# Optimization experiments

Hardware: AMD Instinct MI355X
Metric: run time of the kernel (lower is better)

The kernel has to match this reference:

```python
import jax, jax.numpy as jnp
import numpy as np

N = 10000          # nodes
E = 320000         # edges (avg degree 32)
D_IN = 64          # node_pos feature width
NS, NG, NV = 128, 128, 128   # gate: scalars, gates, gated channels
NTYPES = 8         # edge types
FC = 64            # fc_neurons hidden width
D_OUT = 64
NUM_NEIGHBORS = 32.0


def setup_inputs() -> dict:
    key = jax.random.key(0)
    ks = jax.random.split(key, 32)
    inp = {}
    inp["node_pos"] = jax.random.normal(ks[0], (N, D_IN), dtype=jnp.float32)
    dims_in = [D_IN, D_IN + NS + NV, D_IN + NS + NV]     # 64, 320, 320
    dims_out = [NS + NG + NV, NS + NG + NV, D_OUT]       # 384, 384, 64
    i = 1
    for l in range(3):
        di, do = dims_in[l], dims_out[l]
        inp[f"w_self_{l}"] = jax.random.normal(ks[i], (di, do), dtype=jnp.float32) / np.sqrt(di); i += 1
        inp[f"w_msg_{l}"] = jax.random.normal(ks[i], (di, do), dtype=jnp.float32) / np.sqrt(di); i += 1
        inp[f"fc0_{l}"] = jax.random.normal(ks[i], (NTYPES, FC), dtype=jnp.float32) / np.sqrt(NTYPES); i += 1
        inp[f"fc1_{l}"] = jax.random.normal(ks[i], (FC, FC), dtype=jnp.float32) / np.sqrt(FC); i += 1
        inp[f"fc2_{l}"] = jax.random.normal(ks[i], (FC, do), dtype=jnp.float32) / np.sqrt(FC); i += 1
    inp["edge_src"] = jax.random.randint(ks[i], (E,), 0, N); i += 1
    inp["edge_dst"] = jax.random.randint(ks[i], (E,), 0, N); i += 1
    inp["edge_type"] = jax.random.randint(ks[i], (E,), 0, NTYPES)
    return inp


def _conv(x, edge_src, edge_dst, etype_onehot, w_self, w_msg, f0, f1, f2):
    # fc_neurons MLP on edge attrs -> per-edge tensor-product weights [E, out]
    w = jax.nn.silu(etype_onehot @ f0)
    w = jax.nn.silu(w @ f1)
    w = w @ f2
    # gather source node features, weighted message, scatter-sum to dst
    msg = (x[edge_src] @ w_msg) * w                       # [E, out]
    agg = jax.ops.segment_sum(msg, edge_dst, num_segments=N)
    agg = agg / jnp.sqrt(jnp.asarray(NUM_NEIGHBORS, x.dtype))
    return x @ w_self + agg                               # self-connection + messages


def _gate(h):
    # e3nn Gate: scalars -> silu, gates -> sigmoid, gated channels modulated by gates
    s = h[:, :NS]
    g = h[:, NS:NS + NG]
    v = h[:, NS + NG:]
    return jnp.concatenate([jax.nn.silu(s), v * jax.nn.sigmoid(g)], axis=-1)


def reference(node_pos,
              w_self_0, w_msg_0, fc0_0, fc1_0, fc2_0,
              w_self_1, w_msg_1, fc0_1, fc1_1, fc2_1,
              w_self_2, w_msg_2, fc0_2, fc1_2, fc2_2,
              edge_src, edge_dst, edge_type):
    etype_onehot = jax.nn.one_hot(edge_type, NTYPES, dtype=node_pos.dtype)
    mid = node_pos
    params = [(w_self_0, w_msg_0, fc0_0, fc1_0, fc2_0),
              (w_self_1, w_msg_1, fc0_1, fc1_1, fc2_1)]
    for w_self, w_msg, f0, f1, f2 in params:
        h = _conv(mid, edge_src, edge_dst, etype_onehot, w_self, w_msg, f0, f1, f2)
        mid = jnp.concatenate([node_pos, _gate(h)], axis=-1)   # concated_tensor
    return _conv(mid, edge_src, edge_dst, etype_onehot, w_self_2, w_msg_2, fc0_2, fc1_2, fc2_2)
```

## Files before the change

### kernel.cpp

```cpp
#include <hip/hip_runtime.h>
#include <hip/hip_bf16.h>

#define N_NODES 10000
#define N_EDGES 320000
#define NTYPES 8
#define FC 64
#define SLOTS 96

using short8v = __attribute__((ext_vector_type(8))) short;
using f32x4   = __attribute__((ext_vector_type(4))) float;

__device__ __forceinline__ float sigmoidf_(float x) { return 1.f / (1.f + expf(-x)); }

__device__ __forceinline__ unsigned short f2bf(float x) {
    union { float f; unsigned u; } un; un.f = x;
    unsigned r = un.u + 0x7fff + ((un.u >> 16) & 1);
    return (unsigned short)(r >> 16);
}
__device__ __forceinline__ float bflo(unsigned d) {
    union { unsigned u; float f; } un; un.u = d << 16; return un.f;
}
__device__ __forceinline__ float bfhi(unsigned d) {
    union { unsigned u; float f; } un; un.u = d & 0xffff0000u; return un.f;
}
__device__ __forceinline__ unsigned packbf(float lo, float hi) {
    return (unsigned)f2bf(lo) | ((unsigned)f2bf(hi) << 16);
}

__device__ __forceinline__ void wtrans(const float* __restrict__ in,
                                       unsigned short* __restrict__ out,
                                       int K, int Nn, int idx) {
    int n = idx / K, k = idx - n * K;
    out[idx] = f2bf(in[k * Nn + n]);
}

#define PREP_TOTAL (N_NODES + N_NODES * 64 + 2 * 24576 + 2 * 122880 + 2 * 20480)

__global__ void prep_all(const float* __restrict__ node_pos,
                         const float* __restrict__ w0, const float* __restrict__ w1,
                         const float* __restrict__ w2, const float* __restrict__ w3,
                         const float* __restrict__ w4, const float* __restrict__ w5,
                         const float* __restrict__ f0_0, const float* __restrict__ f1_0,
                         const float* __restrict__ f2_0,
                         const float* __restrict__ f0_1, const float* __restrict__ f1_1,
                         const float* __restrict__ f2_1,
                         const float* __restrict__ f0_2, const float* __restrict__ f1_2,
                         const float* __restrict__ f2_2,
                         int* __restrict__ cnt, unsigned short* __restrict__ np16,
                         unsigned short* __restrict__ o0, unsigned short* __restrict__ o1,
                         unsigned short* __restrict__ o2, unsigned short* __restrict__ o3,
                         unsigned short* __restrict__ o4, unsigned short* __restrict__ o5,
                         float* __restrict__ wtab0, float* __restrict__ wtab1,
                         float* __restrict__ wtab2) {
    const int tid = threadIdx.x;
    const int bb = blockIdx.x;
    if (bb < 26) {
        const float *f0, *f1, *f2;
        float* wtab;
        int dout, idx;
        if (bb < 12)      { f0 = f0_0; f1 = f1_0; f2 = f2_0; wtab = wtab0; dout = 384; idx = bb * 256 + tid; }
        else if (bb < 24) { f0 = f0_1; f1 = f1_1; f2 = f2_1; wtab = wtab1; dout = 384; idx = (bb - 12) * 256 + tid; }
        else              { f0 = f0_2; f1 = f1_2; f2 = f2_2; wtab = wtab2; dout = 64;  idx = (bb - 24) * 256 + tid; }
        __shared__ float a[NTYPES * FC];
        __shared__ float bs[NTYPES * FC];
        for (int i = tid; i < NTYPES * FC; i += 256) { float v = f0[i]; a[i] = v * sigmoidf_(v); }
        __syncthreads();
        for (int i = tid; i < NTYPES * FC; i += 256) {
            int t = i >> 6, j = i & 63;
            float s = 0.f;
            #pragma unroll
            for (int k = 0; k < FC; ++k) s = fmaf(a[t * FC + k], f1[k * FC + j], s);
            bs[i] = s * sigmoidf_(s);
        }
        __syncthreads();
        if (idx >= NTYPES * dout) return;
        int t = idx / dout, c = idx - t * dout;
        float s = 0.f;
        #pragma unroll
        for (int k = 0; k < FC; ++k) s = fmaf(bs[t * FC + k], f2[k * dout + c], s);
        wtab[idx] = s * 0.17677669529663687f;
        return;
    }
    int idx = (bb - 26) * 256 + tid;
    if (idx < N_NODES) { cnt[idx] = 0; return; }
    idx -= N_NODES;
    if (idx < N_NODES * 64) { np16[idx] = f2bf(node_pos[idx]); return; }
    idx -= N_NODES * 64;
    if (idx < 24576) { wtrans(w0, o0, 64, 384, idx); return; }
    idx -= 24576;
    if (idx < 24576) { wtrans(w1, o1, 64, 384, idx); return; }
    idx -= 24576;
    if (idx < 122880) { wtrans(w2, o2, 320, 384, idx); return; }
    idx -= 122880;
    if (idx < 122880) { wtrans(w3, o3, 320, 384, idx); return; }
    idx -= 122880;
    if (idx < 20480) { wtrans(w4, o4, 320, 64, idx); return; }
    idx -= 20480;
    if (idx < 20480) { wtrans(w5, o5, 320, 64, idx); return; }
}

__global__ void fill_kernel(const int* __restrict__ esrc, const int* __restrict__ edst,
                            const int* __restrict__ etype, int* __restrict__ cnt,
                            int* __restrict__ csr) {
    int e4 = (blockIdx.x * 256 + threadIdx.x) * 4;
    if (e4 >= N_EDGES) return;
    int4 s = *reinterpret_cast<const int4*>(&esrc[e4]);
    int4 d = *reinterpret_cast<const int4*>(&edst[e4]);
    int4 t = *reinterpret_cast<const int4*>(&etype[e4]);
    int p;
    p = atomicAdd(&cnt[d.x], 1); if (p < SLOTS) csr[d.x * SLOTS + p] = s.x * 8 + t.x;
    p = atomicAdd(&cnt[d.y], 1); if (p < SLOTS) csr[d.y * SLOTS + p] = s.y * 8 + t.y;
    p = atomicAdd(&cnt[d.z], 1); if (p < SLOTS) csr[d.z * SLOTS + p] = s.z * 8 + t.z;
    p = atomicAdd(&cnt[d.w], 1); if (p < SLOTS) csr[d.w * SLOTS + p] = s.w * 8 + t.w;
}

__global__ __launch_bounds__(256) void mfma_dual(
        const unsigned short* __restrict__ A,
        const unsigned short* __restrict__ BtS, const unsigned short* __restrict__ BtM,
        float* __restrict__ Cs, unsigned short* __restrict__ Cm,
        int M, int K, int N, int nct) {
    int by = blockIdx.y;
    const bool is_msg = (by >= nct);
    const unsigned short* Bt = is_msg ? BtM : BtS;
    if (is_msg) by -= nct;
    const int wave = threadIdx.x >> 6;
    const int lane = threadIdx.x & 63;
    const int r16 = lane & 15;
    const int kg  = lane >> 4;
    const int rowBase = blockIdx.x * 128 + wave * 32;
    const int colBase = by * 64;

    f32x4 acc[2][4] = {};
    for (int k0 = 0; k0 < K; k0 += 32) {
        short8v a[2], b[4];
        #pragma unroll
        for (int mi = 0; mi < 2; ++mi) {
            int r = rowBase + mi * 16 + r16;
            if (r >= M) r = M - 1;
            a[mi] = *reinterpret_cast<const short8v*>(&A[(long long)r * K + k0 + kg * 8]);
        }
        #pragma unroll
        for (int nj = 0; nj < 4; ++nj) {
            int c = colBase + nj * 16 + r16;
            b[nj] = *reinterpret_cast<const short8v*>(&Bt[(long long)c * K + k0 + kg * 8]);
        }
        #pragma unroll
        for (int mi = 0; mi < 2; ++mi)
            #pragma unroll
            for (int nj = 0; nj < 4; ++nj)
                acc[mi][nj] = __builtin_amdgcn_mfma_f32_16x16x32_bf16(
                                  a[mi], b[nj], acc[mi][nj], 0, 0, 0);
    }
    #pragma unroll
    for (int mi = 0; mi < 2; ++mi) {
        #pragma unroll
        for (int j = 0; j < 4; ++j) {
            int r = rowBase + mi * 16 + kg * 4 + j;
            if (r >= M) continue;
            #pragma unroll
            for (int nj = 0; nj < 4; ++nj) {
                int c = colBase + nj * 16 + r16;
                float v = acc[mi][nj][j];
                if (is_msg) Cm[(long long)r * N + c] = f2bf(v);
                else        Cs[(long long)r * N + c] = v;
            }
        }
    }
}

__global__ __launch_bounds__(512) void gather_gate(
        const unsigned short* __restrict__ ymsg,
        const float* __restrict__ yself,
        const unsigned short* __restrict__ np16,
        const float* __restrict__ wtab,
        const int* __restrict__ cnt,
        const int* __restrict__ csr,
        unsigned short* __restrict__ mid16) {
    __shared__ float wt[NTYPES * 384];
    __shared__ float sacc[4][6][64];
    const int tid = threadIdx.x;
    for (int i = tid; i < NTYPES * 384; i += 512) wt[i] = wtab[i];
    const int wv = tid >> 6;
    const int lane = tid & 63;
    const int nib = wv >> 1;
    const int sub = wv & 1;
    const int node = blockIdx.x * 4 + nib;
    int deg = cnt[node];
    if (deg > SLOTS) deg = SLOTS;
    int h = (((deg + 1) >> 1) + 3) & ~3;
    if (h > deg) h = deg;
    const int e0 = sub ? h : 0;
    const int e1 = sub ? deg : h;
    const int* __restrict__ row = csr + node * SLOTS;
    const unsigned* __restrict__ y32 = (const unsigned*)ymsg;
    const float2* __restrict__ wt2 = (const float2*)wt;
    __syncthreads();

    float acc[3][2] = {};
    int i = e0;
    for (; i + 3 < e1; i += 4) {
        int4 p = *reinterpret_cast<const int4*>(&row[i]);
        unsigned b0 = (unsigned)(p.x >> 3) * 192u + lane, t0 = (unsigned)(p.x & 7) * 192u + lane;
        unsigned b1 = (unsigned)(p.y >> 3) * 192u + lane, t1 = (unsigned)(p.y & 7) * 192u + lane;
        unsigned b2 = (unsigned)(p.z >> 3) * 192u + lane, t2 = (unsigned)(p.z & 7) * 192u + lane;
        unsigned b3 = (unsigned)(p.w >> 3) * 192u + lane, t3 = (unsigned)(p.w & 7) * 192u + lane;
        #pragma unroll
        for (int j = 0; j < 3; ++j) {
            const unsigned o = j * 64;
            unsigned d0 = y32[b0 + o]; float2 w0 = wt2[t0 + o];
            unsigned d1 = y32[b1 + o]; float2 w1 = wt2[t1 + o];
            unsigned d2 = y32[b2 + o]; float2 w2 = wt2[t2 + o];
            unsigned d3 = y32[b3 + o]; float2 w3 = wt2[t3 + o];
            acc[j][0] = fmaf(bflo(d0), w0.x, acc[j][0]);
            acc[j][1] = fmaf(bfhi(d0), w0.y, acc[j][1]);
            acc[j][0] = fmaf(bflo(d1), w1.x, acc[j][0]);
            acc[j][1] = fmaf(bfhi(d1), w1.y, acc[j][1]);
            acc[j][0] = fmaf(bflo(d2), w2.x, acc[j][0]);
            acc[j][1] = fmaf(bfhi(d2), w2.y, acc[j][1]);
            acc[j][0] = fmaf(bflo(d3), w3.x, acc[j][0]);
            acc[j][1] = fmaf(bfhi(d3), w3.y, acc[j][1]);
        }
    }
    for (; i < e1; ++i) {
        int p0 = row[i];
        unsigned b0 = (unsigned)(p0 >> 3) * 192u + lane, t0 = (unsigned)(p0 & 7) * 192u + lane;
        #pragma unroll
        for (int j = 0; j < 3; ++j) {
            unsigned d0 = y32[b0 + j * 64]; float2 w0 = wt2[t0 + j * 64];
            acc[j][0] = fmaf(bflo(d0), w0.x, acc[j][0]);
            acc[j][1] = fmaf(bfhi(d0), w0.y, acc[j][1]);
        }
    }
    if (sub == 1) {
        #pragma unroll
        for (int j = 0; j < 3; ++j) {
            sacc[nib][2 * j][lane]     = acc[j][0];
            sacc[nib][2 * j + 1][lane] = acc[j][1];
        }
    }
    __syncthreads();
    if (sub == 1) return;
    const float2* __restrict__ ysv = (const float2*)(yself + (long long)node * 384);
    float h2[3][2];
    #pragma unroll
    for (int j = 0; j < 3; ++j) {
        float2 ys = ysv[j * 64 + lane];
        h2[j][0] = ys.x + acc[j][0] + sacc[nib][2 * j][lane];
        h2[j][1] = ys.y + acc[j][1] + sacc[nib][2 * j + 1][lane];
    }
    unsigned* __restrict__ m32 = (unsigned*)(mid16 + (long long)node * 320);
    const unsigned* __restrict__ np32 = (const unsigned*)np16;
    if (lane < 32) m32[lane] = np32[node * 32 + lane];
    m32[32 + lane] = packbf(h2[0][0] * sigmoidf_(h2[0][0]),
                            h2[0][1] * sigmoidf_(h2[0][1]));
    m32[96 + lane] = packbf(h2[2][0] * sigmoidf_(h2[1][0]),
                            h2[2][1] * sigmoidf_(h2[1][1]));
}

__global__ void gather_final(const unsigned short* __restrict__ ymsg,
                             const float* __restrict__ yself,
                             const float* __restrict__ wtab,
                             const int* __restrict__ cnt,
                             const int* __restrict__ csr,
                             float* __restrict__ out) {
    __shared__ float wt[NTYPES * 64];
    const int tid = threadIdx.x;
    for (int i = tid; i < NTYPES * 64; i += 256) wt[i] = wtab[i];
    __syncthreads();
    const int node = blockIdx.x * 4 + (tid >> 6);
    const int lane = tid & 63;
    if (node >= N_NODES) return;
    int deg = cnt[node];
    if (deg > SLOTS) deg = SLOTS;
    const int* __restrict__ row = csr + node * SLOTS;
    const unsigned* __restrict__ y32 = (const unsigned*)ymsg;
    const float2* __restrict__ wt2 = (const float2*)wt;
    const int half = lane >> 5, cl = lane & 31;
    float a0 = 0.f, a1 = 0.f;
    int i = 0;
    for (; i + 7 < deg; i += 8) {
        #pragma unroll
        for (int q = 0; q < 4; ++q) {
            int p = row[i + 2 * q + half];
            unsigned d = y32[(unsigned)(p >> 3) * 32u + cl];
            float2 w = wt2[(unsigned)(p & 7) * 32u + cl];
            a0 = fmaf(bflo(d), w.x, a0);
            a1 = fmaf(bfhi(d), w.y, a1);
        }
    }
    for (; i + 1 < deg; i += 2) {
        int p = row[i + half];
        unsigned d = y32[(unsigned)(p >> 3) * 32u + cl];
        float2 w = wt2[(unsigned)(p & 7) * 32u + cl];
        a0 = fmaf(bflo(d), w.x, a0);
        a1 = fmaf(bfhi(d), w.y, a1);
    }
    if (i < deg) {
        if (half == 0) {
            int p = row[i];
            unsigned d = y32[(unsigned)(p >> 3) * 32u + cl];
            float2 w = wt2[(unsigned)(p & 7) * 32u + cl];
            a0 = fmaf(bflo(d), w.x, a0);
            a1 = fmaf(bfhi(d), w.y, a1);
        }
    }
    a0 += __shfl_xor(a0, 32);
    a1 += __shfl_xor(a1, 32);
    if (half == 0) {
        float2 o;
        o.x = yself[(long long)node * 64 + 2 * cl]     + a0;
        o.y = yself[(long long)node * 64 + 2 * cl + 1] + a1;
        reinterpret_cast<float2*>(out)[(long long)node * 32 + cl] = o;
    }
}

extern "C" void kernel_launch(void* const* d_in, const int* in_sizes, int n_in,
                              void* d_out, int out_size, void* d_ws, size_t ws_size,
                              hipStream_t stream) {
    const float* node_pos = (const float*)d_in[0];
    const float* w_self[3] = {(const float*)d_in[1], (const float*)d_in[6],  (const float*)d_in[11]};
    const float* w_msg[3]  = {(const float*)d_in[2], (const float*)d_in[7],  (const float*)d_in[12]};
    const float* fc0[3]    = {(const float*)d_in[3], (const float*)d_in[8],  (const float*)d_in[13]};
    const float* fc1[3]    = {(const float*)d_in[4], (const float*)d_in[9],  (const float*)d_in[14]};
    const float* fc2[3]    = {(const float*)d_in[5], (const float*)d_in[10], (const float*)d_in[15]};
    const int* esrc  = (const int*)d_in[16];
    const int* edst  = (const int*)d_in[17];
    const int* etype = (const int*)d_in[18];
    float* out = (float*)d_out;

    float* f = (float*)d_ws;
    float* wtab0 = f; f += NTYPES * 384;
    float* wtab1 = f; f += NTYPES * 384;
    float* wtab2 = f; f += NTYPES * 64;
    float* yself = f; f += (long long)N_NODES * 384;
    unsigned short* u = (unsigned short*)f;
    unsigned short* ymsg16 = u; u += (long long)N_NODES * 384;
    unsigned short* mid16  = u; u += (long long)N_NODES * 320;
    unsigned short* np16   = u; u += (long long)N_NODES * 64;
    unsigned short* bt0s = u; u += 64 * 384;
    unsigned short* bt0m = u; u += 64 * 384;
    unsigned short* bt1s = u; u += 320 * 384;
    unsigned short* bt1m = u; u += 320 * 384;
    unsigned short* bt2s = u; u += 320 * 64;
    unsigned short* bt2m = u; u += 320 * 64;
    int* ip = (int*)u;
    int* cnt = ip; ip += N_NODES;
    int* csr = ip; ip += (long long)N_NODES * SLOTS;

    prep_all<<<26 + (PREP_TOTAL + 255) / 256, 256, 0, stream>>>(
        node_pos, w_self[0], w_msg[0], w_self[1], w_msg[1], w_self[2], w_msg[2],
        fc0[0], fc1[0], fc2[0], fc0[1], fc1[1], fc2[1], fc0[2], fc1[2], fc2[2],
        cnt, np16, bt0s, bt0m, bt1s, bt1m, bt2s, bt2m, wtab0, wtab1, wtab2);

    fill_kernel<<<(N_EDGES / 4 + 255) / 256, 256, 0, stream>>>(esrc, edst, etype, cnt, csr);

    const int mrows = (N_NODES + 127) / 128;
    const int ggrid = N_NODES / 4;

    {
        dim3 g(mrows, 2 * (384 / 64));
        mfma_dual<<<g, 256, 0, stream>>>(np16, bt0s, bt0m, yself, ymsg16,
                                         N_NODES, 64, 384, 384 / 64);
        gather_gate<<<ggrid, 512, 0, stream>>>(ymsg16, yself, np16, wtab0, cnt, csr, mid16);
    }
    {
        dim3 g(mrows, 2 * (384 / 64));
        mfma_dual<<<g, 256, 0, stream>>>(mid16, bt1s, bt1m, yself, ymsg16,
                                         N_NODES, 320, 384, 384 / 64);
        gather_gate<<<ggrid, 512, 0, stream>>>(ymsg16, yself, np16, wtab1, cnt, csr, mid16);
    }
    {
        dim3 g(mrows, 2 * (64 / 64));
        mfma_dual<<<g, 256, 0, stream>>>(mid16, bt2s, bt2m, yself, ymsg16,
                                         N_NODES, 320, 64, 64 / 64);
        gather_final<<<(N_NODES + 3) / 4, 256, 0, stream>>>(ymsg16, yself, wtab2, cnt, csr, out);
    }
}
```

Baseline: 171.2 us.

## Fuse CSR fill with layer-0 GEMM and compute self/msg GEMMs together

The edge-bucketing fill kernel and the first layer's dual GEMM now run in one launch, with the blocks split between the two tasks so they can overlap. A new dual-output GEMM block computes the self and message projections in the same block, so each A tile is loaded once for both. The node_pos columns of the concatenated mid buffer are written once during prep instead of by every gather_gate call. The cost is more registers per thread for the two accumulator sets, and fewer blocks in the fused GEMM grid.

```diff
diff --git a/kernel.cpp b/kernel.cpp
--- a/kernel.cpp
+++ b/kernel.cpp
@@ -6,6 +6,8 @@
 #define NTYPES 8
 #define FC 64
 #define SLOTS 96
+#define FILLB 313
+#define MROWS 79
 
 using short8v = __attribute__((ext_vector_type(8))) short;
 using f32x4   = __attribute__((ext_vector_type(4))) float;
@@ -34,7 +36,7 @@
     out[idx] = f2bf(in[k * Nn + n]);
 }
 
-#define PREP_TOTAL (N_NODES + N_NODES * 64 + 2 * 24576 + 2 * 122880 + 2 * 20480)
+#define PREP_TOTAL (N_NODES + N_NODES * 32 + N_NODES * 32 + 2 * 24576 + 2 * 122880 + 2 * 20480)
 
 __global__ void prep_all(const float* __restrict__ node_pos,
                          const float* __restrict__ w0, const float* __restrict__ w1,
@@ -47,6 +49,7 @@
                          const float* __restrict__ f0_2, const float* __restrict__ f1_2,
                          const float* __restrict__ f2_2,
                          int* __restrict__ cnt, unsigned short* __restrict__ np16,
+                         unsigned short* __restrict__ mid16,
                          unsigned short* __restrict__ o0, unsigned short* __restrict__ o1,
                          unsigned short* __restrict__ o2, unsigned short* __restrict__ o3,
                          unsigned short* __restrict__ o4, unsigned short* __restrict__ o5,
@@ -84,8 +87,19 @@
     int idx = (bb - 26) * 256 + tid;
     if (idx < N_NODES) { cnt[idx] = 0; return; }
     idx -= N_NODES;
-    if (idx < N_NODES * 64) { np16[idx] = f2bf(node_pos[idx]); return; }
-    idx -= N_NODES * 64;
+    if (idx < N_NODES * 32) {
+        unsigned* np32 = (unsigned*)np16;
+        np32[idx] = packbf(node_pos[idx * 2], node_pos[idx * 2 + 1]);
+        return;
+    }
+    idx -= N_NODES * 32;
+    if (idx < N_NODES * 32) {
+        int node = idx >> 5, j = idx & 31;
+        unsigned* m32 = (unsigned*)(mid16 + (long long)node * 320);
+        m32[j] = packbf(node_pos[node * 64 + 2 * j], node_pos[node * 64 + 2 * j + 1]);
+        return;
+    }
+    idx -= N_NODES * 32;
     if (idx < 24576) { wtrans(w0, o0, 64, 384, idx); return; }
     idx -= 24576;
     if (idx < 24576) { wtrans(w1, o1, 64, 384, idx); return; }
@@ -99,40 +113,22 @@
     if (idx < 20480) { wtrans(w5, o5, 320, 64, idx); return; }
 }
 
-__global__ void fill_kernel(const int* __restrict__ esrc, const int* __restrict__ edst,
-                            const int* __restrict__ etype, int* __restrict__ cnt,
-                            int* __restrict__ csr) {
-    int e4 = (blockIdx.x * 256 + threadIdx.x) * 4;
-    if (e4 >= N_EDGES) return;
-    int4 s = *reinterpret_cast<const int4*>(&esrc[e4]);
-    int4 d = *reinterpret_cast<const int4*>(&edst[e4]);
-    int4 t = *reinterpret_cast<const int4*>(&etype[e4]);
-    int p;
-    p = atomicAdd(&cnt[d.x], 1); if (p < SLOTS) csr[d.x * SLOTS + p] = s.x * 8 + t.x;
-    p = atomicAdd(&cnt[d.y], 1); if (p < SLOTS) csr[d.y * SLOTS + p] = s.y * 8 + t.y;
-    p = atomicAdd(&cnt[d.z], 1); if (p < SLOTS) csr[d.z * SLOTS + p] = s.z * 8 + t.z;
-    p = atomicAdd(&cnt[d.w], 1); if (p < SLOTS) csr[d.w * SLOTS + p] = s.w * 8 + t.w;
-}
-
-__global__ __launch_bounds__(256) void mfma_dual(
+__device__ __forceinline__ void gemm_dual_block(
         const unsigned short* __restrict__ A,
         const unsigned short* __restrict__ BtS, const unsigned short* __restrict__ BtM,
         float* __restrict__ Cs, unsigned short* __restrict__ Cm,
-        int M, int K, int N, int nct) {
-    int by = blockIdx.y;
-    const bool is_msg = (by >= nct);
-    const unsigned short* Bt = is_msg ? BtM : BtS;
-    if (is_msg) by -= nct;
-    const int wave = threadIdx.x >> 6;
-    const int lane = threadIdx.x & 63;
+        int M, int K, int N, int bx, int by, int tid) {
+    const int wave = tid >> 6;
+    const int lane = tid & 63;
     const int r16 = lane & 15;
     const int kg  = lane >> 4;
-    const int rowBase = blockIdx.x * 128 + wave * 32;
+    const int rowBase = bx * 128 + wave * 32;
     const int colBase = by * 64;
 
-    f32x4 acc[2][4] = {};
+    f32x4 accS[2][4] = {};
+    f32x4 accM[2][4] = {};
     for (int k0 = 0; k0 < K; k0 += 32) {
-        short8v a[2], b[4];
+        short8v a[2], bS[4], bM[4];
         #pragma unroll
         for (int mi = 0; mi < 2; ++mi) {
             int r = rowBase + mi * 16 + r16;
@@ -142,14 +138,18 @@
         #pragma unroll
         for (int nj = 0; nj < 4; ++nj) {
             int c = colBase + nj * 16 + r16;
-            b[nj] = *reinterpret_cast<const short8v*>(&Bt[(long long)c * K + k0 + kg * 8]);
+            bS[nj] = *reinterpret_cast<const short8v*>(&BtS[(long long)c * K + k0 + kg * 8]);
+            bM[nj] = *reinterpret_cast<const short8v*>(&BtM[(long long)c * K + k0 + kg * 8]);
         }
         #pragma unroll
         for (int mi = 0; mi < 2; ++mi)
             #pragma unroll
-            for (int nj = 0; nj < 4; ++nj)
-                acc[mi][nj] = __builtin_amdgcn_mfma_f32_16x16x32_bf16(
-                                  a[mi], b[nj], acc[mi][nj], 0, 0, 0);
+            for (int nj = 0; nj < 4; ++nj) {
+                accS[mi][nj] = __builtin_amdgcn_mfma_f32_16x16x32_bf16(
+                                   a[mi], bS[nj], accS[mi][nj], 0, 0, 0);
+                accM[mi][nj] = __builtin_amdgcn_mfma_f32_16x16x32_bf16(
+                                   a[mi], bM[nj], accM[mi][nj], 0, 0, 0);
+            }
     }
     #pragma unroll
     for (int mi = 0; mi < 2; ++mi) {
@@ -160,18 +160,50 @@
             #pragma unroll
             for (int nj = 0; nj < 4; ++nj) {
                 int c = colBase + nj * 16 + r16;
-                float v = acc[mi][nj][j];
-                if (is_msg) Cm[(long long)r * N + c] = f2bf(v);
-                else        Cs[(long long)r * N + c] = v;
+                Cs[(long long)r * N + c] = accS[mi][nj][j];
+                Cm[(long long)r * N + c] = f2bf(accM[mi][nj][j]);
             }
         }
     }
+}
+
+__global__ __launch_bounds__(256) void mfma_dual2(
+        const unsigned short* __restrict__ A,
+        const unsigned short* __restrict__ BtS, const unsigned short* __restrict__ BtM,
+        float* __restrict__ Cs, unsigned short* __restrict__ Cm,
+        int M, int K, int N) {
+    gemm_dual_block(A, BtS, BtM, Cs, Cm, M, K, N, blockIdx.x, blockIdx.y, threadIdx.x);
+}
+
+__global__ __launch_bounds__(256) void fill_gemm0(
+        const int* __restrict__ esrc, const int* __restrict__ edst,
+        const int* __restrict__ etype, int* __restrict__ cnt,
+        int* __restrict__ csr,
+        const unsigned short* __restrict__ A,
+        const unsigned short* __restrict__ BtS, const unsigned short* __restrict__ BtM,
+        float* __restrict__ Cs, unsigned short* __restrict__ Cm) {
+    const int bb = blockIdx.x;
+    if (bb < FILLB) {
+        int e4 = (bb * 256 + threadIdx.x) * 4;
+        if (e4 >= N_EDGES) return;
+        int4 s = *reinterpret_cast<const int4*>(&esrc[e4]);
+        int4 d = *reinterpret_cast<const int4*>(&edst[e4]);
+        int4 t = *reinterpret_cast<const int4*>(&etype[e4]);
+        int p;
+        p = atomicAdd(&cnt[d.x], 1); if (p < SLOTS) csr[d.x * SLOTS + p] = s.x * 8 + t.x;
+        p = atomicAdd(&cnt[d.y], 1); if (p < SLOTS) csr[d.y * SLOTS + p] = s.y * 8 + t.y;
+        p = atomicAdd(&cnt[d.z], 1); if (p < SLOTS) csr[d.z * SLOTS + p] = s.z * 8 + t.z;
+        p = atomicAdd(&cnt[d.w], 1); if (p < SLOTS) csr[d.w * SLOTS + p] = s.w * 8 + t.w;
+        return;
+    }
+    int gb = bb - FILLB;
+    gemm_dual_block(A, BtS, BtM, Cs, Cm, N_NODES, 64, 384,
+                    gb % MROWS, gb / MROWS, threadIdx.x);
 }
 
 __global__ __launch_bounds__(512) void gather_gate(
         const unsigned short* __restrict__ ymsg,
         const float* __restrict__ yself,
-        const unsigned short* __restrict__ np16,
         const float* __restrict__ wtab,
         const int* __restrict__ cnt,
         const int* __restrict__ csr,
@@ -249,12 +281,64 @@
         h2[j][1] = ys.y + acc[j][1] + sacc[nib][2 * j + 1][lane];
     }
     unsigned* __restrict__ m32 = (unsigned*)(mid16 + (long long)node * 320);
-    const unsigned* __restrict__ np32 = (const unsigned*)np16;
-    if (lane < 32) m32[lane] = np32[node * 32 + lane];
     m32[32 + lane] = packbf(h2[0][0] * sigmoidf_(h2[0][0]),
                             h2[0][1] * sigmoidf_(h2[0][1]));
     m32[96 + lane] = packbf(h2[2][0] * sigmoidf_(h2[1][0]),
                             h2[2][1] * sigmoidf_(h2[1][1]));
+}
+
+__global__ __launch_bounds__(256) void mfma_dual(
+        const unsigned short* __restrict__ A,
+        const unsigned short* __restrict__ BtS, const unsigned short* __restrict__ BtM,
+        float* __restrict__ Cs, unsigned short* __restrict__ Cm,
+        int M, int K, int N, int nct) {
+    int by = blockIdx.y;
+    const bool is_msg = (by >= nct);
+    const unsigned short* Bt = is_msg ? BtM : BtS;
+    if (is_msg) by -= nct;
+    const int wave = threadIdx.x >> 6;
+    const int lane = threadIdx.x & 63;
+    const int r16 = lane & 15;
+    const int kg  = lane >> 4;
+    const int rowBase = blockIdx.x * 128 + wave * 32;
+    const int colBase = by * 64;
+
+    f32x4 acc[2][4] = {};
+    for (int k0 = 0; k0 < K; k0 += 32) {
+        short8v a[2], b[4];
+        #pragma unroll
+        for (int mi = 0; mi < 2; ++mi) {
+            int r = rowBase + mi * 16 + r16;
+            if (r >= M) r = M - 1;
+            a[mi] = *reinterpret_cast<const short8v*>(&A[(long long)r * K + k0 + kg * 8]);
+        }
+        #pragma unroll
+        for (int nj = 0; nj < 4; ++nj) {
+            int c = colBase + nj * 16 + r16;
+            b[nj] = *reinterpret_cast<const short8v*>(&Bt[(long long)c * K + k0 + kg * 8]);
+        }
+        #pragma unroll
+        for (int mi = 0; mi < 2; ++mi)
+            #pragma unroll
+            for (int nj = 0; nj < 4; ++nj)
+                acc[mi][nj] = __builtin_amdgcn_mfma_f32_16x16x32_bf16(
+                                  a[mi], b[nj], acc[mi][nj], 0, 0, 0);
+    }
+    #pragma unroll
+    for (int mi = 0; mi < 2; ++mi) {
+        #pragma unroll
+        for (int j = 0; j < 4; ++j) {
+            int r = rowBase + mi * 16 + kg * 4 + j;
+            if (r >= M) continue;
+            #pragma unroll
+            for (int nj = 0; nj < 4; ++nj) {
+                int c = colBase + nj * 16 + r16;
+                float v = acc[mi][nj][j];
+                if (is_msg) Cm[(long long)r * N + c] = f2bf(v);
+                else        Cs[(long long)r * N + c] = v;
+            }
+        }
+    }
 }
 
 __global__ void gather_final(const unsigned short* __restrict__ ymsg,
@@ -350,29 +434,24 @@
     prep_all<<<26 + (PREP_TOTAL + 255) / 256, 256, 0, stream>>>(
         node_pos, w_self[0], w_msg[0], w_self[1], w_msg[1], w_self[2], w_msg[2],
         fc0[0], fc1[0], fc2[0], fc0[1], fc1[1], fc2[1], fc0[2], fc1[2], fc2[2],
-        cnt, np16, bt0s, bt0m, bt1s, bt1m, bt2s, bt2m, wtab0, wtab1, wtab2);
-
-    fill_kernel<<<(N_EDGES / 4 + 255) / 256, 256, 0, stream>>>(esrc, edst, etype, cnt, csr);
-
-    const int mrows = (N_NODES + 127) / 128;
+        cnt, np16, mid16, bt0s, bt0m, bt1s, bt1m, bt2s, bt2m, wtab0, wtab1, wtab2);
+
     const int ggrid = N_NODES / 4;
 
+    fill_gemm0<<<FILLB + MROWS * 6, 256, 0, stream>>>(
+        esrc, edst, etype, cnt, csr, np16, bt0s, bt0m, yself, ymsg16);
+    gather_gate<<<ggrid, 512, 0, stream>>>(ymsg16, yself, wtab0, cnt, csr, mid16);
+
     {
-        dim3 g(mrows, 2 * (384 / 64));
-        mfma_dual<<<g, 256, 0, stream>>>(np16, bt0s, bt0m, yself, ymsg16,
-                                         N_NODES, 64, 384, 384 / 64);
-        gather_gate<<<ggrid, 512, 0, stream>>>(ymsg16, yself, np16, wtab0, cnt, csr, mid16);
+        dim3 g(MROWS, 384 / 64);
+        mfma_dual2<<<g, 256, 0, stream>>>(mid16, bt1s, bt1m, yself, ymsg16,
+                                          N_NODES, 320, 384);
+        gather_gate<<<ggrid, 512, 0, stream>>>(ymsg16, yself, wtab1, cnt, csr, mid16);
     }
     {
-        dim3 g(mrows, 2 * (384 / 64));
-        mfma_dual<<<g, 256, 0, stream>>>(mid16, bt1s, bt1m, yself, ymsg16,
-                                         N_NODES, 320, 384, 384 / 64);
-        gather_gate<<<ggrid, 512, 0, stream>>>(ymsg16, yself, np16, wtab1, cnt, csr, mid16);
-    }
-    {
-        dim3 g(mrows, 2 * (64 / 64));
+        dim3 g(MROWS, 2);
         mfma_dual<<<g, 256, 0, stream>>>(mid16, bt2s, bt2m, yself, ymsg16,
-                                         N_NODES, 320, 64, 64 / 64);
+                                         N_NODES, 320, 64, 1);
         gather_final<<<(N_NODES + 3) / 4, 256, 0, stream>>>(ymsg16, yself, wtab2, cnt, csr, out);
     }
 }
```

Result: faster. 160.5 us (-6.3%).
